# Kernel optimization log

Measured on AMD Instinct MI355X. Metric: run time of the kernel, lower is better.

The kernel has to match this reference:

```python
import jax, jax.numpy as jnp
import numpy as np

LATENT = 100
INIT_SIZE = 8   # img_size // 4
NUM = 200       # LIF time steps
BETA = 0.95
THR = 1.0
CH_OUT = 3

# snntorch ATan surrogate spike (alpha=2 -> grad = 1/(1+(pi*u)^2))
@jax.custom_vjp
def spike_fn(x):
    return (x > 0).astype(x.dtype)

def _spike_fwd(x):
    return (x > 0).astype(x.dtype), x

def _spike_bwd(x, g):
    return (g / (1.0 + (jnp.pi * x) ** 2),)

spike_fn.defvjp(_spike_fwd, _spike_bwd)

def batchnorm(x, gamma, beta, eps):
    # training-mode BN: batch statistics over (N,H,W), biased variance (as torch)
    mean = x.mean(axis=(0, 2, 3), keepdims=True)
    var = ((x - mean) ** 2).mean(axis=(0, 2, 3), keepdims=True)
    xh = (x - mean) * jax.lax.rsqrt(var + eps)
    return xh * gamma[None, :, None, None] + beta[None, :, None, None]

def upsample2x(x):  # nearest-neighbor, scale 2
    return jnp.repeat(jnp.repeat(x, 2, axis=2), 2, axis=3)

def conv2d(x, w, b):  # 3x3, stride 1, padding 1
    y = jax.lax.conv_general_dilated(x, w, (1, 1), [(1, 1), (1, 1)],
                                     dimension_numbers=("NCHW", "OIHW", "NCHW"))
    return y + b[None, :, None, None]

def leaky_relu(x):
    return jnp.where(x >= 0, x, 0.2 * x)

def setup_inputs() -> dict:
    key = jax.random.key(0)
    ks = jax.random.split(key, 8)
    B = 8
    def n(k, shape, s=0.02):
        return jax.random.normal(k, shape, dtype=jnp.float32) * s
    return {
        "z": jax.random.normal(ks[0], (B, LATENT), dtype=jnp.float32),
        "w_l1": n(ks[1], (LATENT, 128 * INIT_SIZE ** 2)),
        "b_l1": jnp.zeros((128 * INIT_SIZE ** 2,), jnp.float32),
        "g1": jnp.ones((128,), jnp.float32), "be1": jnp.zeros((128,), jnp.float32),
        "w_c1": n(ks[2], (128, NUM * 128, 3, 3), 0.005),
        "b_c1": jnp.zeros((128,), jnp.float32),
        "g2": jnp.ones((128,), jnp.float32), "be2": jnp.zeros((128,), jnp.float32),
        "w_c2": n(ks[3], (64, 128, 3, 3)),
        "b_c2": jnp.zeros((64,), jnp.float32),
        "g3": jnp.ones((64,), jnp.float32), "be3": jnp.zeros((64,), jnp.float32),
        "w_c3": n(ks[4], (CH_OUT, 64, 3, 3)),
        "b_c3": jnp.zeros((CH_OUT,), jnp.float32),
    }

def reference(z, w_l1, b_l1, g1, be1, w_c1, b_c1, g2, be2, w_c2, b_c2, g3, be3, w_c3, b_c3):
    B = z.shape[0]
    out = z @ w_l1 + b_l1                       # (B, 128*8*8)
    out = out.reshape(B, 128, INIT_SIZE, INIT_SIZE)
    out = batchnorm(out, g1, be1, 1e-5)
    out = upsample2x(out)                       # (B,128,16,16) constant LIF input

    def lif_step(mem, _):
        # snntorch Leaky, reset-by-subtraction; reset detached from grad
        reset = jax.lax.stop_gradient((mem > THR).astype(mem.dtype))
        mem = BETA * mem + out - reset * THR
        spk = spike_fn(mem - THR)
        return mem, spk

    mem0 = jnp.zeros_like(out)
    _, spk_rec = jax.lax.scan(lif_step, mem0, None, length=NUM)  # (NUM,B,128,16,16)
    # faithful to torch.stack(dim=0).reshape(B, -1, 16, 16)
    x = spk_rec.reshape(B, NUM * 128, 16, 16)
    x = conv2d(x, w_c1, b_c1)                   # (B,128,16,16)
    x = leaky_relu(batchnorm(x, g2, be2, 0.8))  # BatchNorm2d(128, 0.8): eps=0.8
    x = upsample2x(x)                           # (B,128,32,32)
    x = conv2d(x, w_c2, b_c2)                   # (B,64,32,32)
    x = leaky_relu(batchnorm(x, g3, be3, 0.8))
    x = conv2d(x, w_c3, b_c3)                   # (B,3,32,32)
    return jnp.tanh(x)
```

## Files before the change

kernel.cpp:

```cpp
#include <hip/hip_runtime.h>
#include <math.h>


#define WROW 25632
#define SROW 25664

typedef _Float16 half8 __attribute__((ext_vector_type(8)));
typedef float f32x4 __attribute__((ext_vector_type(4)));
typedef unsigned int uint4v __attribute__((ext_vector_type(4)));

union AFrag { uint4v u4; unsigned int u[4]; half8 h; };

__global__ __launch_bounds__(256) void k_lin_bn1(
    const float* __restrict__ z, const float* __restrict__ w,
    const float* __restrict__ bias, const float* __restrict__ g1,
    const float* __restrict__ be1, float* __restrict__ I) {
  int ch = blockIdx.x, tid = threadIdx.x;
  __shared__ float red[256];
  int hw = tid & 63, b0 = tid >> 6;
  int j = ch * 64 + hw;
  float acc0 = bias[j], acc1 = acc0;
  const float* zp0 = z + b0 * 100;
  const float* zp1 = z + (b0 + 4) * 100;
  for (int l = 0; l < 100; ++l) {
    float wv = w[l * 8192 + j];
    acc0 += zp0[l] * wv;
    acc1 += zp1[l] * wv;
  }
  float v0 = acc0, v1 = acc1;
  red[tid] = v0 + v1; __syncthreads();
  for (int s = 128; s > 0; s >>= 1) { if (tid < s) red[tid] += red[tid + s]; __syncthreads(); }
  float mean = red[0] * (1.0f / 512.0f);
  __syncthreads();
  float d0 = v0 - mean, d1 = v1 - mean;
  red[tid] = d0 * d0 + d1 * d1; __syncthreads();
  for (int s = 128; s > 0; s >>= 1) { if (tid < s) red[tid] += red[tid + s]; __syncthreads(); }
  float var = red[0] * (1.0f / 512.0f);
  float coef = g1[ch] / sqrtf(var + 1e-5f);
  float beta = be1[ch];
  float q0 = (v0 - mean) * coef + beta;
  float q1 = (v1 - mean) * coef + beta;
#pragma unroll
  for (int k = 0; k < 2; ++k) {
    int n = k ? (tid + 256) : tid; float q = k ? q1 : q0;
    int b = n >> 6, hh = n & 63, h = hh >> 3, ww = hh & 7;
    float* o = I + (size_t)(b * 128 + ch) * 256 + (2 * h) * 16 + 2 * ww;
    o[0] = q; o[1] = q; o[16] = q; o[17] = q;
  }
}

__global__ __launch_bounds__(256) void k_lif(
    const float* __restrict__ I, unsigned char* __restrict__ spkTb) {
  int g = blockIdx.x * 256 + threadIdx.x;
  if (g < 217600) {
    int hr = g / 3200;
    int i  = g - hr * 3200;
    int row;
    if (hr < 18)      row = hr;
    else if (hr < 36) row = 306 + (hr - 18);
    else { int kk = hr - 36; row = ((kk >> 1) + 1) * 18 + ((kk & 1) ? 17 : 0); }
    *(unsigned long long*)(spkTb + (size_t)row * SROW + (size_t)i * 8) = 0ULL;
  }
  int px = g >> 10, plane = g & 1023;
  int lane = threadIdx.x & 63;
  float in = I[plane * 256 + px];
  int pos = ((px >> 4) + 1) * 18 + (px & 15) + 1;
  unsigned long long* wsrow =
      (unsigned long long*)(spkTb + (size_t)pos * SROW + ((plane - lane) >> 3));
  float mem = 0.0f;
  for (int t = 0; t < 200; ++t) {
    float reset = (mem > 1.0f) ? 1.0f : 0.0f;
    mem = 0.95f * mem + in - reset;
    unsigned long long m = __ballot(mem > 1.0f);
    if (lane == 0) wsrow[t * 16] = m;
  }
}

__global__ __launch_bounds__(256) void k_wtrans(
    const float* __restrict__ wc1, _Float16* __restrict__ wT) {
  __shared__ float t[2][2304];
  int op = blockIdx.x / 100, cg = blockIdx.x % 100;
  int oc0 = op * 2, c0 = cg * 256, tid = threadIdx.x;
  const float* src = wc1 + (size_t)oc0 * 230400 + (size_t)c0 * 9;
#pragma unroll
  for (int i = 0; i < 9; ++i) {
    t[0][tid + i * 256] = src[tid + i * 256];
    t[1][tid + i * 256] = src[230400 + tid + i * 256];
  }
  __syncthreads();
  int oh = tid >> 7;
  int cp = tid & 127;
#pragma unroll
  for (int tap = 0; tap < 9; ++tap) {
    union { unsigned int u; _Float16 h[2]; } pk;
    pk.h[0] = (_Float16)t[oh][(2 * cp) * 9 + tap];
    pk.h[1] = (_Float16)t[oh][(2 * cp + 1) * 9 + tap];
    *(unsigned int*)((char*)wT +
        ((size_t)(tap * 128 + oc0 + oh) * WROW + c0 + 2 * cp) * 2) = pk.u;
  }
}

__device__ inline void expandp(unsigned int b, AFrag& f) {
  unsigned int lo = ((b & 0xFu) * 0x00204081u) & 0x01010101u;
  unsigned int hi = ((b >> 4) * 0x00204081u) & 0x01010101u;
  lo *= 0x3Cu; hi *= 0x3Cu;
  f.u[0] = __builtin_amdgcn_perm(0u, lo, 0x01040004u);
  f.u[1] = __builtin_amdgcn_perm(0u, lo, 0x03040204u);
  f.u[2] = __builtin_amdgcn_perm(0u, hi, 0x01040004u);
  f.u[3] = __builtin_amdgcn_perm(0u, hi, 0x03040204u);
}

__device__ __forceinline__ void gll16(const void* g, void* l) {
  __builtin_amdgcn_global_load_lds(
      (const __attribute__((address_space(1))) unsigned int*)g,
      (__attribute__((address_space(3))) unsigned int*)l, 16, 0, 0);
}

__global__ __launch_bounds__(256, 3) void k_conv1_mfma(
    const unsigned char* __restrict__ spkTb, const _Float16* __restrict__ wT,
    _Float16* __restrict__ y1p) {
  int v = (blockIdx.x & 7) * 96 + (blockIdx.x >> 3);
  int sl = v >> 4;
  int r = v & 15;
  int half = r >> 3, b = r & 7;
  int tid = threadIdx.x;
  int wave = tid >> 6, lane = tid & 63;
  int quad = lane >> 4, l16 = lane & 15;
  int qs = quad * 8;
  int h0 = wave * 4;

  int q0 = (sl * 25) / 6;
  int qc = ((sl + 1) * 25) / 6 - q0;
  int NBS = 9 * qc;

  __shared__ _Float16 As[2][8192];

  int ocl = tid >> 4;
  int sc0 = (tid & 15) ^ ocl;
  const char* srcA0 = (const char*)wT + (size_t)q0 * 256
                    + (size_t)(half * 64 + ocl) * (WROW * 2) + sc0 * 16;

  const unsigned char* rowp[4];
#pragma unroll
  for (int nt = 0; nt < 4; ++nt)
    rowp[nt] = spkTb + b * 3200 + q0 * 16
             + (size_t)((h0 + nt) * 18 + l16) * SROW;

  int dsb[4];
#pragma unroll
  for (int s = 0; s < 4; ++s)
    dsb[s] = l16 * 256 + ((s * 64 + quad * 16) ^ (l16 << 4));

  f32x4 acc[4][4] = {};
  uint4v bx[4], bxn[4];

#pragma unroll
  for (int i = 0; i < 4; ++i)
    gll16(srcA0 + (size_t)i * (16 * WROW * 2), (char*)As + i * 4096 + wave * 1024);
#pragma unroll
  for (int nt = 0; nt < 4; ++nt)
    bx[nt] = *(const uint4v*)(rowp[nt]);
  __syncthreads();

  size_t atap = 0;
  int btap = 0, dw = 0;
  int qi = 0;
  for (int k = 0; k < NBS; ++k) {
    int qin = qi + 1;
    size_t atapn = atap; int btapn = btap; int dwn = dw;
    if (qin == qc) {
      qin = 0;
      atapn = atap + (size_t)128 * (WROW * 2);
      btapn = btap + ((dw == 2) ? 16 * SROW : SROW);
      dwn = (dw == 2) ? 0 : dw + 1;
    }
    if (k + 1 < NBS) {
      int bo = btapn + qin * 16;
#pragma unroll
      for (int nt = 0; nt < 4; ++nt)
        bxn[nt] = *(const uint4v*)(rowp[nt] + bo);
      const char* sA = srcA0 + atapn + (size_t)(qin * 256);
      char* dst = (char*)As + ((k + 1) & 1) * 16384 + wave * 1024;
#pragma unroll
      for (int i = 0; i < 4; ++i)
        gll16(sA + (size_t)i * (16 * WROW * 2), dst + i * 4096);
    }
    const char* cA = (const char*)As + (k & 1) * 16384;
#pragma unroll
    for (int s = 0; s < 4; ++s) {
      AFrag a[4];
#pragma unroll
      for (int mt = 0; mt < 4; ++mt)
        a[mt].u4 = *(const uint4v*)(cA + dsb[s] + mt * 4096);
#pragma unroll
      for (int nt = 0; nt < 4; ++nt) {
        AFrag bf; expandp((bx[nt][s] >> qs) & 0xFFu, bf);
#pragma unroll
        for (int mt = 0; mt < 4; ++mt)
          acc[mt][nt] = __builtin_amdgcn_mfma_f32_16x16x32_f16(
              a[mt].h, bf.h, acc[mt][nt], 0, 0, 0);
      }
    }
    __syncthreads();
    if (k + 1 < NBS) {
#pragma unroll
      for (int nt = 0; nt < 4; ++nt) bx[nt] = bxn[nt];
    }
    qi = qin; atap = atapn; btap = btapn; dw = dwn;
  }

  _Float16* ob = y1p + (size_t)(sl * 8 + b) * 32768 + half * 16384;
#pragma unroll
  for (int mt = 0; mt < 4; ++mt)
#pragma unroll
    for (int nt = 0; nt < 4; ++nt) {
      int px = (h0 + nt) * 16 + l16;
#pragma unroll
      for (int rr = 0; rr < 4; ++rr) {
        int oc = mt * 16 + quad * 4 + rr;
        ob[(size_t)oc * 256 + px] = (_Float16)acc[mt][nt][rr];
      }
    }
}

__global__ __launch_bounds__(256) void k_bn2_up(
    const _Float16* __restrict__ y1p, const float* __restrict__ bc1,
    const float* __restrict__ g2, const float* __restrict__ be2,
    float* __restrict__ x2p) {
  int ch = blockIdx.x, tid = threadIdx.x;
  __shared__ float red[256];

  for (int e = tid; e < 1056; e += 256) {
    int b = e / 132, i = e - b * 132;
    int rr, cc;
    if (i < 34)       { rr = 0;       cc = i; }
    else if (i < 68)  { rr = 33;      cc = i - 34; }
    else if (i < 100) { rr = i - 67;  cc = 0; }
    else              { rr = i - 99;  cc = 33; }
    x2p[(size_t)(b * 128 + ch) * 1156 + rr * 34 + cc] = 0.0f;
  }

  int pp = tid & 127;
  int bh = tid >> 7;
  float bias = bc1[ch];
  float a[4][2] = {};
  const char* base = (const char*)y1p + ((size_t)ch * 256 + pp * 2) * 2
                   + (size_t)bh * 4 * 65536;
  for (int tl = 0; tl < 48; ++tl) {
    const char* q = base + (size_t)tl * 524288;
#pragma unroll
    for (int k = 0; k < 4; ++k) {
      union { unsigned int u; _Float16 h[2]; } cv;
      cv.u = *(const unsigned int*)(q + (size_t)k * 65536);
      a[k][0] += (float)cv.h[0];
      a[k][1] += (float)cv.h[1];
    }
  }
  float vv[4][2]; float s = 0.0f;
#pragma unroll
  for (int k = 0; k < 4; ++k)
#pragma unroll
    for (int e = 0; e < 2; ++e) { vv[k][e] = a[k][e] + bias; s += vv[k][e]; }

  red[tid] = s; __syncthreads();
  for (int st = 128; st > 0; st >>= 1) { if (tid < st) red[tid] += red[tid + st]; __syncthreads(); }
  float mean = red[0] * (1.0f / 2048.0f);
  __syncthreads();
  s = 0.0f;
#pragma unroll
  for (int k = 0; k < 4; ++k)
#pragma unroll
    for (int e = 0; e < 2; ++e) { float d = vv[k][e] - mean; s += d * d; }
  red[tid] = s; __syncthreads();
  for (int st = 128; st > 0; st >>= 1) { if (tid < st) red[tid] += red[tid + st]; __syncthreads(); }
  float var = red[0] * (1.0f / 2048.0f);
  float coef = g2[ch] / sqrtf(var + 0.8f);
  float beta = be2[ch];
#pragma unroll
  for (int k = 0; k < 4; ++k)
#pragma unroll
    for (int e = 0; e < 2; ++e) {
      int b = bh * 4 + k, px = pp * 2 + e, h = px >> 4, w = px & 15;
      float q = (vv[k][e] - mean) * coef + beta;
      q = (q >= 0.0f) ? q : 0.2f * q;
      float* o = x2p + (size_t)(b * 128 + ch) * 1156 + (2 * h + 1) * 34 + (2 * w + 1);
      o[0] = q; o[1] = q; o[34] = q; o[35] = q;
    }
}

__global__ __launch_bounds__(256) void k_conv2(
    const float* __restrict__ x2p, const float* __restrict__ wc2,
    const float* __restrict__ bc2, float* __restrict__ y2) {
  int octile = blockIdx.x, b = blockIdx.y, pq = blockIdx.z;
  int tid = threadIdx.x;
  int p = pq * 256 + tid, h = p >> 5, w = p & 31;
  float a0 = 0.0f, a1 = 0.0f, a2 = 0.0f, a3 = 0.0f;
  const float* base = x2p + (size_t)(b * 128) * 1156 + h * 34 + w;
  const float* wb = wc2 + (size_t)(octile * 4) * 128 * 9;
  for (int ch = 0; ch < 128; ++ch) {
    const float* pp = base + (size_t)ch * 1156;
    float s0 = pp[0],  s1 = pp[1],  s2 = pp[2];
    float s3 = pp[34], s4 = pp[35], s5 = pp[36];
    float s6 = pp[68], s7 = pp[69], s8 = pp[70];
    const float* w0 = wb + (size_t)ch * 9;
    const float* w1 = wb + (size_t)(128 + ch) * 9;
    const float* w2 = wb + (size_t)(256 + ch) * 9;
    const float* w3 = wb + (size_t)(384 + ch) * 9;
    a0 += s0*w0[0]+s1*w0[1]+s2*w0[2]+s3*w0[3]+s4*w0[4]+s5*w0[5]+s6*w0[6]+s7*w0[7]+s8*w0[8];
    a1 += s0*w1[0]+s1*w1[1]+s2*w1[2]+s3*w1[3]+s4*w1[4]+s5*w1[5]+s6*w1[6]+s7*w1[7]+s8*w1[8];
    a2 += s0*w2[0]+s1*w2[1]+s2*w2[2]+s3*w2[3]+s4*w2[4]+s5*w2[5]+s6*w2[6]+s7*w2[7]+s8*w2[8];
    a3 += s0*w3[0]+s1*w3[1]+s2*w3[2]+s3*w3[3]+s4*w3[4]+s5*w3[5]+s6*w3[6]+s7*w3[7]+s8*w3[8];
  }
  int oc0 = octile * 4;
  y2[(size_t)(b * 64 + oc0 + 0) * 1024 + p] = a0 + bc2[oc0 + 0];
  y2[(size_t)(b * 64 + oc0 + 1) * 1024 + p] = a1 + bc2[oc0 + 1];
  y2[(size_t)(b * 64 + oc0 + 2) * 1024 + p] = a2 + bc2[oc0 + 2];
  y2[(size_t)(b * 64 + oc0 + 3) * 1024 + p] = a3 + bc2[oc0 + 3];
}

__global__ __launch_bounds__(256) void k_bn3(
    const float* __restrict__ y2, const float* __restrict__ g3,
    const float* __restrict__ be3, float* __restrict__ y2n) {
  int ch = blockIdx.x, tid = threadIdx.x;
  __shared__ float red[256];

  for (int e = tid; e < 1056; e += 256) {
    int b = e / 132, i = e - b * 132;
    int rr, cc;
    if (i < 34)       { rr = 0;       cc = i; }
    else if (i < 68)  { rr = 33;      cc = i - 34; }
    else if (i < 100) { rr = i - 67;  cc = 0; }
    else              { rr = i - 99;  cc = 33; }
    y2n[(size_t)(b * 64 + ch) * 1156 + rr * 34 + cc] = 0.0f;
  }

  float v[32]; float s = 0.0f;
#pragma unroll
  for (int k = 0; k < 32; ++k) {
    int n = tid + k * 256;
    v[k] = y2[(size_t)((n >> 10) * 64 + ch) * 1024 + (n & 1023)];
    s += v[k];
  }
  red[tid] = s; __syncthreads();
  for (int st = 128; st > 0; st >>= 1) { if (tid < st) red[tid] += red[tid + st]; __syncthreads(); }
  float mean = red[0] * (1.0f / 8192.0f);
  __syncthreads();
  s = 0.0f;
#pragma unroll
  for (int k = 0; k < 32; ++k) { float d = v[k] - mean; s += d * d; }
  red[tid] = s; __syncthreads();
  for (int st = 128; st > 0; st >>= 1) { if (tid < st) red[tid] += red[tid + st]; __syncthreads(); }
  float var = red[0] * (1.0f / 8192.0f);
  float coef = g3[ch] / sqrtf(var + 0.8f);
  float beta = be3[ch];
#pragma unroll
  for (int k = 0; k < 32; ++k) {
    int n = tid + k * 256;
    int b = n >> 10, px = n & 1023, h = px >> 5, w = px & 31;
    float q = (v[k] - mean) * coef + beta;
    q = (q >= 0.0f) ? q : 0.2f * q;
    y2n[(size_t)(b * 64 + ch) * 1156 + (h + 1) * 34 + (w + 1)] = q;
  }
}

__global__ __launch_bounds__(256) void k_conv3(
    const float* __restrict__ y2n, const float* __restrict__ wc3,
    const float* __restrict__ bc3, float* __restrict__ out) {
  int b = blockIdx.x >> 4, pg = blockIdx.x & 15;
  int tid = threadIdx.x;
  int pxl = tid & 63, cg = tid >> 6;
  int p = pg * 64 + pxl, h = p >> 5, w = p & 31;
  float a0 = 0.0f, a1 = 0.0f, a2 = 0.0f;
  const float* base = y2n + (size_t)(b * 64 + cg * 16) * 1156 + h * 34 + w;
  for (int c = 0; c < 16; ++c) {
    int ch = cg * 16 + c;
    const float* pp = base + (size_t)c * 1156;
    float s0 = pp[0],  s1 = pp[1],  s2 = pp[2];
    float s3 = pp[34], s4 = pp[35], s5 = pp[36];
    float s6 = pp[68], s7 = pp[69], s8 = pp[70];
    const float* w0 = wc3 + (size_t)ch * 9;
    const float* w1 = wc3 + (size_t)(64 + ch) * 9;
    const float* w2 = wc3 + (size_t)(128 + ch) * 9;
    a0 += s0*w0[0]+s1*w0[1]+s2*w0[2]+s3*w0[3]+s4*w0[4]+s5*w0[5]+s6*w0[6]+s7*w0[7]+s8*w0[8];
    a1 += s0*w1[0]+s1*w1[1]+s2*w1[2]+s3*w1[3]+s4*w1[4]+s5*w1[5]+s6*w1[6]+s7*w1[7]+s8*w1[8];
    a2 += s0*w2[0]+s1*w2[1]+s2*w2[2]+s3*w2[3]+s4*w2[4]+s5*w2[5]+s6*w2[6]+s7*w2[7]+s8*w2[8];
  }
  __shared__ float red[3][256];
  red[0][tid] = a0; red[1][tid] = a1; red[2][tid] = a2;
  __syncthreads();
  if (tid < 192) {
    int oc = tid >> 6, px = tid & 63;
    float sres = red[oc][px] + red[oc][px + 64] + red[oc][px + 128] + red[oc][px + 192];
    out[(size_t)(b * 3 + oc) * 1024 + pg * 64 + px] = tanhf(sres + bc3[oc]);
  }
}

extern "C" void kernel_launch(void* const* d_in, const int* in_sizes, int n_in,
                              void* d_out, int out_size, void* d_ws, size_t ws_size,
                              hipStream_t stream) {
  const float* z    = (const float*)d_in[0];
  const float* w_l1 = (const float*)d_in[1];
  const float* b_l1 = (const float*)d_in[2];
  const float* g1   = (const float*)d_in[3];
  const float* be1  = (const float*)d_in[4];
  const float* w_c1 = (const float*)d_in[5];
  const float* b_c1 = (const float*)d_in[6];
  const float* g2   = (const float*)d_in[7];
  const float* be2  = (const float*)d_in[8];
  const float* w_c2 = (const float*)d_in[9];
  const float* b_c2 = (const float*)d_in[10];
  const float* g3   = (const float*)d_in[11];
  const float* be3  = (const float*)d_in[12];
  const float* w_c3 = (const float*)d_in[13];
  const float* b_c3 = (const float*)d_in[14];
  float* out = (float*)d_out;

  char* ws = (char*)d_ws;
  _Float16* wT = (_Float16*)ws;
  unsigned char* spkTb = (unsigned char*)(ws + 59056128);
  float* I   = (float*)(ws + 67633408);
  _Float16* y1p = (_Float16*)(ws + 69730560);
  float* x2p = (float*)ws;
  float* y2n = (float*)(ws + 4734976);
  float* y2  = (float*)(ws + 7102464);

  k_wtrans <<<6400, 256, 0, stream>>>(w_c1, wT);
  k_lin_bn1<<<128, 256, 0, stream>>>(z, w_l1, b_l1, g1, be1, I);
  k_lif    <<<1024, 256, 0, stream>>>(I, spkTb);
  k_conv1_mfma<<<768, 256, 0, stream>>>(spkTb, wT, y1p);

  k_bn2_up <<<128, 256, 0, stream>>>(y1p, b_c1, g2, be2, x2p);
  k_conv2  <<<dim3(16, 8, 4), 256, 0, stream>>>(x2p, w_c2, b_c2, y2);
  k_bn3    <<<64, 256, 0, stream>>>(y2, g3, be3, y2n);
  k_conv3  <<<128, 256, 0, stream>>>(y2n, w_c3, b_c3, out);
}
```

Measured before the change: 436.1 us.

## Load spike B-fragments in-iteration and remap conv2/conv3 block indices by batch

In the conv1 MFMA kernel, the register double-buffering of the spike (B) fragments is dropped. Each iteration now loads its B rows directly, computing the offset from a tap index rather than from incrementally tracked offsets. This cuts register pressure and address bookkeeping, but exposes the global load latency at the start of each iteration. Separately, conv2 and conv3 are launched on a 1D grid whose lowest index bits select the batch element, which changes which blocks run together and how they share the cache.

```diff
diff --git a/kernel.cpp b/kernel.cpp
--- a/kernel.cpp
+++ b/kernel.cpp
@@ -152,38 +152,28 @@
     dsb[s] = l16 * 256 + ((s * 64 + quad * 16) ^ (l16 << 4));
 
   f32x4 acc[4][4] = {};
-  uint4v bx[4], bxn[4];
 
 #pragma unroll
   for (int i = 0; i < 4; ++i)
     gll16(srcA0 + (size_t)i * (16 * WROW * 2), (char*)As + i * 4096 + wave * 1024);
-#pragma unroll
-  for (int nt = 0; nt < 4; ++nt)
-    bx[nt] = *(const uint4v*)(rowp[nt]);
-  __syncthreads();
-
-  size_t atap = 0;
-  int btap = 0, dw = 0;
-  int qi = 0;
+  __syncthreads();
+
+  int tap = 0, qi = 0;
   for (int k = 0; k < NBS; ++k) {
-    int qin = qi + 1;
-    size_t atapn = atap; int btapn = btap; int dwn = dw;
-    if (qin == qc) {
-      qin = 0;
-      atapn = atap + (size_t)128 * (WROW * 2);
-      btapn = btap + ((dw == 2) ? 16 * SROW : SROW);
-      dwn = (dw == 2) ? 0 : dw + 1;
-    }
+    int dh = tap / 3, dw = tap - dh * 3;
+    uint4v bx[4];
+    int boff = (dh * 18 + dw) * SROW + qi * 16;
+#pragma unroll
+    for (int nt = 0; nt < 4; ++nt)
+      bx[nt] = *(const uint4v*)(rowp[nt] + boff);
+    int qin = qi + 1, tapn = tap;
+    if (qin == qc) { qin = 0; tapn = tap + 1; }
     if (k + 1 < NBS) {
-      int bo = btapn + qin * 16;
-#pragma unroll
-      for (int nt = 0; nt < 4; ++nt)
-        bxn[nt] = *(const uint4v*)(rowp[nt] + bo);
-      const char* sA = srcA0 + atapn + (size_t)(qin * 256);
+      size_t aoff = (size_t)tapn * ((size_t)128 * WROW * 2) + (size_t)qin * 256;
       char* dst = (char*)As + ((k + 1) & 1) * 16384 + wave * 1024;
 #pragma unroll
       for (int i = 0; i < 4; ++i)
-        gll16(sA + (size_t)i * (16 * WROW * 2), dst + i * 4096);
+        gll16(srcA0 + (size_t)i * (16 * WROW * 2) + aoff, dst + i * 4096);
     }
     const char* cA = (const char*)As + (k & 1) * 16384;
 #pragma unroll
@@ -202,11 +192,7 @@
       }
     }
     __syncthreads();
-    if (k + 1 < NBS) {
-#pragma unroll
-      for (int nt = 0; nt < 4; ++nt) bx[nt] = bxn[nt];
-    }
-    qi = qin; atap = atapn; btap = btapn; dw = dwn;
+    tap = tapn; qi = qin;
   }
 
   _Float16* ob = y1p + (size_t)(sl * 8 + b) * 32768 + half * 16384;
@@ -291,7 +277,9 @@
 __global__ __launch_bounds__(256) void k_conv2(
     const float* __restrict__ x2p, const float* __restrict__ wc2,
     const float* __restrict__ bc2, float* __restrict__ y2) {
-  int octile = blockIdx.x, b = blockIdx.y, pq = blockIdx.z;
+  int b = blockIdx.x & 7;
+  int rem = blockIdx.x >> 3;
+  int octile = rem >> 2, pq = rem & 3;
   int tid = threadIdx.x;
   int p = pq * 256 + tid, h = p >> 5, w = p & 31;
   float a0 = 0.0f, a1 = 0.0f, a2 = 0.0f, a3 = 0.0f;
@@ -366,7 +354,7 @@
 __global__ __launch_bounds__(256) void k_conv3(
     const float* __restrict__ y2n, const float* __restrict__ wc3,
     const float* __restrict__ bc3, float* __restrict__ out) {
-  int b = blockIdx.x >> 4, pg = blockIdx.x & 15;
+  int b = blockIdx.x & 7, pg = blockIdx.x >> 3;
   int tid = threadIdx.x;
   int pxl = tid & 63, cg = tid >> 6;
   int p = pg * 64 + pxl, h = p >> 5, w = p & 31;
@@ -430,7 +418,7 @@
   k_conv1_mfma<<<768, 256, 0, stream>>>(spkTb, wT, y1p);
 
   k_bn2_up <<<128, 256, 0, stream>>>(y1p, b_c1, g2, be2, x2p);
-  k_conv2  <<<dim3(16, 8, 4), 256, 0, stream>>>(x2p, w_c2, b_c2, y2);
+  k_conv2  <<<512, 256, 0, stream>>>(x2p, w_c2, b_c2, y2);
   k_bn3    <<<64, 256, 0, stream>>>(y2, g3, be3, y2n);
   k_conv3  <<<128, 256, 0, stream>>>(y2n, w_c3, b_c3, out);
 }
```

After: 430.8 us. No clear change (-1.2%).
